# Optimization experiments

Measured on AMD Instinct MI355X. Metric: run time of the kernel, lower is better.

The kernel has to match this reference:

```python
import jax, jax.numpy as jnp
import numpy as np

EPS = 1e-08
MARGIN = 0.5
B, D = 512, 768
N_CLASSES = 7


def setup_inputs() -> dict:
    key = jax.random.key(0)
    k1, k2 = jax.random.split(key)
    embeddings = jax.random.normal(k1, (B, D), dtype=jnp.float32)
    labels = jax.random.randint(k2, (B,), 0, N_CLASSES, dtype=jnp.int64)
    return {"embeddings": embeddings, "labels": labels}


def _cosine_distance_matrix(x):
    # 1 - x_i . x_j / (max(||x_i||, eps) * max(||x_j||, eps))  (torch cosine_similarity semantics)
    norms = jnp.maximum(jnp.linalg.norm(x, axis=-1, keepdims=True), EPS)
    xn = x / norms
    return 1.0 - xn @ xn.T  # (B, B)


def _triplet_mask(labels):
    n = labels.shape[0]
    ne = ~jnp.eye(n, dtype=bool)  # indices not equal
    distinct = ne[:, :, None] & ne[:, None, :] & ne[None, :, :]  # i!=j, i!=k, j!=k
    lbl_eq = labels[None, :] == labels[:, None]  # (B, B)
    valid = lbl_eq[:, :, None] & ~lbl_eq[:, None, :]  # label[i]==label[j], label[i]!=label[k]
    return distinct & valid


def reference(embeddings, labels):
    dist = _cosine_distance_matrix(embeddings)  # (B, B)
    # triplet_loss[i, j, k] = d(i, j) - d(i, k) + margin
    tl = dist[:, :, None] - dist[:, None, :] + MARGIN  # (B, B, B)
    mask = _triplet_mask(labels)
    tl = jax.nn.relu(tl * mask.astype(tl.dtype))
    num_pos = jnp.sum((tl > EPS).astype(jnp.float32))
    return jnp.sum(tl) / (num_pos + EPS)
```

## Files before the change

### kernel.cpp

```cpp
#include <hip/hip_runtime.h>

#define EPSF 1e-8f
#define MARGINF 0.5f
#define BN 512
#define DD 768
#define BT 64
#define SPLITK 8
#define KC (DD / SPLITK)
#define LPAD 104
#define NORMBLK 128

typedef __attribute__((ext_vector_type(8))) short bf16x8;
typedef __attribute__((ext_vector_type(4))) float f32x4;

__device__ __forceinline__ short f2bf(float f) {
    unsigned int u = __float_as_uint(f);
    return (short)((u + 0x7FFFu + ((u >> 16) & 1u)) >> 16);
}

__device__ __forceinline__ bf16x8 pack8(const float4& a, const float4& b) {
    bf16x8 r;
    r[0] = f2bf(a.x); r[1] = f2bf(a.y); r[2] = f2bf(a.z); r[3] = f2bf(a.w);
    r[4] = f2bf(b.x); r[5] = f2bf(b.y); r[6] = f2bf(b.z); r[7] = f2bf(b.w);
    return r;
}

__global__ __launch_bounds__(256) void prep_kernel(const float* __restrict__ x,
                                                   float* __restrict__ invn,
                                                   float* __restrict__ dotp) {
    int b = blockIdx.x;
    int t = threadIdx.x;
    int wv = t >> 6, lane = t & 63;

    if (b >= BN) {
        int row = (b - BN) * 4 + wv;
        float s = 0.f;
#pragma unroll
        for (int c = 0; c < 3; ++c) {
            float4 v = *(const float4*)&x[row * DD + (lane + c * 64) * 4];
            s += v.x * v.x + v.y * v.y + v.z * v.z + v.w * v.w;
        }
        for (int off = 32; off; off >>= 1) s += __shfl_down(s, off, 64);
        if (lane == 0) invn[row] = 1.0f / fmaxf(sqrtf(s), EPSF);
        return;
    }

    __shared__ __align__(16) short As[BT][LPAD];
    __shared__ __align__(16) short Bs[BT][LPAD];
    int bz = b >> 6, bi = (b >> 3) & 7, bj = b & 7;
    int i0 = bi * BT, j0 = bj * BT, kbase = bz * KC;

    {
        int row = t >> 2, fq = t & 3;
        const float* ap = &x[(i0 + row) * DD + kbase + fq * 8];
        const float* bp = &x[(j0 + row) * DD + kbase + fq * 8];
#pragma unroll
        for (int cc = 0; cc < 3; ++cc) {
            float4 a0 = *(const float4*)(ap + cc * 32);
            float4 a1 = *(const float4*)(ap + cc * 32 + 4);
            float4 b0 = *(const float4*)(bp + cc * 32);
            float4 b1 = *(const float4*)(bp + cc * 32 + 4);
            *(bf16x8*)&As[row][fq * 8 + cc * 32] = pack8(a0, a1);
            *(bf16x8*)&Bs[row][fq * 8 + cc * 32] = pack8(b0, b1);
        }
    }
    __syncthreads();

    int r16 = lane & 15;
    int kb8 = (lane >> 4) * 8;

    f32x4 accf[4];
#pragma unroll
    for (int c = 0; c < 4; ++c) accf[c] = (f32x4){0.f, 0.f, 0.f, 0.f};

#pragma unroll
    for (int s = 0; s < 3; ++s) {
        bf16x8 af = *(const bf16x8*)&As[wv * 16 + r16][kb8 + s * 32];
#pragma unroll
        for (int c = 0; c < 4; ++c) {
            bf16x8 bf_ = *(const bf16x8*)&Bs[c * 16 + r16][kb8 + s * 32];
            accf[c] = __builtin_amdgcn_mfma_f32_16x16x32_bf16(af, bf_, accf[c], 0, 0, 0);
        }
    }

    float* o = dotp + (size_t)bz * BN * BN;
    int crow = i0 + wv * 16 + (lane >> 4) * 4;
#pragma unroll
    for (int c = 0; c < 4; ++c) {
        int ccol = j0 + c * 16 + r16;
#pragma unroll
        for (int r = 0; r < 4; ++r)
            o[(crow + r) * BN + ccol] = accf[c][r];
    }
}

__global__ __launch_bounds__(256) void triplet_kernel(const float* __restrict__ dotp,
                                                      const float* __restrict__ invn,
                                                      const int* __restrict__ labels,
                                                      float* __restrict__ psum,
                                                      unsigned int* __restrict__ pcnt) {
    int i = blockIdx.x;
    int t = threadIdx.x;
    int w = t >> 6, lane = t & 63;
    __shared__ float drow[BN];
    __shared__ int lab[BN];
    __shared__ __align__(16) float dpos[528];
    __shared__ int wcnt[8];
    __shared__ int woff[9];
    __shared__ float redf[4];
    __shared__ unsigned int redc[4];

    lab[t] = labels[t];
    lab[t + 256] = labels[t + 256];
    float inv_i = invn[i];
#pragma unroll
    for (int e0 = 0; e0 < BN; e0 += 256) {
        int e = e0 + t;
        float s = 0.f;
#pragma unroll
        for (int z = 0; z < SPLITK; ++z) s += dotp[(size_t)z * BN * BN + i * BN + e];
        drow[e] = 1.0f - s * inv_i * invn[e];
    }
    __syncthreads();

    int li = lab[i];
    bool p0 = (lab[t] == li) && (t != i);
    bool p1 = (lab[t + 256] == li) && ((t + 256) != i);
    unsigned long long m0 = __ballot(p0);
    unsigned long long m1 = __ballot(p1);
    if (lane == 0) { wcnt[w] = __popcll(m0); wcnt[4 + w] = __popcll(m1); }
    __syncthreads();
    if (t == 0) {
        int s = 0;
#pragma unroll
        for (int q = 0; q < 8; ++q) { woff[q] = s; s += wcnt[q]; }
        woff[8] = s;
    }
    __syncthreads();
    unsigned long long lmask = (1ull << lane) - 1ull;
    if (p0) dpos[woff[w] + __popcll(m0 & lmask)] = drow[t] + MARGINF;
    if (p1) dpos[woff[4 + w] + __popcll(m1 & lmask)] = drow[t + 256] + MARGINF;
    int npos = woff[8];
    int npad = (npos + 15) & ~15;
    if (t < npad - npos) dpos[npos + t] = -1e30f;
    __syncthreads();

    float dk0 = (lab[t] != li) ? drow[t] : 1e30f;
    float dk1 = (lab[t + 256] != li) ? drow[t + 256] : 1e30f;
    float sum = 0.f;
    unsigned int cnt = 0;
    for (int n = 0; n < npad; n += 16) {
        float4 q[4];
#pragma unroll
        for (int v = 0; v < 4; ++v) q[v] = *(const float4*)&dpos[n + v * 4];
#pragma unroll
        for (int v = 0; v < 4; ++v) {
            float bv[4] = {q[v].x, q[v].y, q[v].z, q[v].w};
#pragma unroll
            for (int u = 0; u < 4; ++u) {
                float v0 = bv[u] - dk0;
                float v1 = bv[u] - dk1;
                sum += fmaxf(v0, 0.f);
                if (v0 > EPSF) cnt++;
                sum += fmaxf(v1, 0.f);
                if (v1 > EPSF) cnt++;
            }
        }
    }
    for (int off = 32; off; off >>= 1) {
        sum += __shfl_down(sum, off, 64);
        cnt += __shfl_down(cnt, off, 64);
    }
    if (lane == 0) { redf[w] = sum; redc[w] = cnt; }
    __syncthreads();
    if (t == 0) {
        psum[i] = redf[0] + redf[1] + redf[2] + redf[3];
        pcnt[i] = redc[0] + redc[1] + redc[2] + redc[3];
    }
}

__global__ __launch_bounds__(256) void reduce_kernel(const float* __restrict__ psum,
                                                     const unsigned int* __restrict__ pcnt,
                                                     float* __restrict__ out) {
    int t = threadIdx.x;
    double s = (double)psum[t] + (double)psum[t + 256];
    double c = (double)pcnt[t] + (double)pcnt[t + 256];
    for (int off = 32; off; off >>= 1) {
        s += __shfl_down(s, off, 64);
        c += __shfl_down(c, off, 64);
    }
    __shared__ double sred[4], cred[4];
    if ((t & 63) == 0) { sred[t >> 6] = s; cred[t >> 6] = c; }
    __syncthreads();
    if (t == 0) {
        double stot = sred[0] + sred[1] + sred[2] + sred[3];
        double ctot = cred[0] + cred[1] + cred[2] + cred[3];
        out[0] = (float)(stot / (ctot + 1e-8));
    }
}

extern "C" void kernel_launch(void* const* d_in, const int* in_sizes, int n_in,
                              void* d_out, int out_size, void* d_ws, size_t ws_size,
                              hipStream_t stream) {
    const float* x = (const float*)d_in[0];
    const int* labels = (const int*)d_in[1];
    float* out = (float*)d_out;

    char* ws = (char*)d_ws;
    float* invn = (float*)(ws + 256);
    float* psum = (float*)(ws + 4096);
    unsigned int* pcnt = (unsigned int*)(ws + 8192);
    float* dotp = (float*)(ws + 16384);

    prep_kernel<<<BN + NORMBLK, 256, 0, stream>>>(x, invn, dotp);
    triplet_kernel<<<BN, 256, 0, stream>>>(dotp, invn, labels, psum, pcnt);
    reduce_kernel<<<1, 256, 0, stream>>>(psum, pcnt, out);
}
```

Before: 19.42 us.

## Replace split-K Gram partials with full-K 64x64 tiles in 1024-thread blocks

The Gram matrix kernel no longer splits K across 8 slices written to separate partial buffers. Each of 64 blocks of 1024 threads now loops over the full K dimension in 128-wide chunks and writes one final dot product per element. The triplet kernel then reads a single row instead of summing 8 partials, which cuts global write and read traffic by about 8x. The cost is far less GEMM parallelism (64 blocks instead of 512) and a serial K loop with two barriers per chunk and no prefetch overlap.

```diff
diff --git a/kernel.cpp b/kernel.cpp
--- a/kernel.cpp
+++ b/kernel.cpp
@@ -5,10 +5,11 @@
 #define BN 512
 #define DD 768
 #define BT 64
-#define SPLITK 8
-#define KC (DD / SPLITK)
-#define LPAD 104
-#define NORMBLK 128
+#define GBLK 64
+#define NBLK 32
+#define CHK 128
+#define NCHK 6
+#define LP 136
 
 typedef __attribute__((ext_vector_type(8))) short bf16x8;
 typedef __attribute__((ext_vector_type(4))) float f32x4;
@@ -25,15 +26,15 @@
     return r;
 }
 
-__global__ __launch_bounds__(256) void prep_kernel(const float* __restrict__ x,
-                                                   float* __restrict__ invn,
-                                                   float* __restrict__ dotp) {
+__global__ __launch_bounds__(1024) void prep_kernel(const float* __restrict__ x,
+                                                    float* __restrict__ invn,
+                                                    float* __restrict__ dist) {
     int b = blockIdx.x;
     int t = threadIdx.x;
     int wv = t >> 6, lane = t & 63;
 
-    if (b >= BN) {
-        int row = (b - BN) * 4 + wv;
+    if (b >= GBLK) {
+        int row = (b - GBLK) * 16 + wv;
         float s = 0.f;
 #pragma unroll
         for (int c = 0; c < 3; ++c) {
@@ -45,56 +46,45 @@
         return;
     }
 
-    __shared__ __align__(16) short As[BT][LPAD];
-    __shared__ __align__(16) short Bs[BT][LPAD];
-    int bz = b >> 6, bi = (b >> 3) & 7, bj = b & 7;
-    int i0 = bi * BT, j0 = bj * BT, kbase = bz * KC;
-
-    {
-        int row = t >> 2, fq = t & 3;
-        const float* ap = &x[(i0 + row) * DD + kbase + fq * 8];
-        const float* bp = &x[(j0 + row) * DD + kbase + fq * 8];
-#pragma unroll
-        for (int cc = 0; cc < 3; ++cc) {
-            float4 a0 = *(const float4*)(ap + cc * 32);
-            float4 a1 = *(const float4*)(ap + cc * 32 + 4);
-            float4 b0 = *(const float4*)(bp + cc * 32);
-            float4 b1 = *(const float4*)(bp + cc * 32 + 4);
-            *(bf16x8*)&As[row][fq * 8 + cc * 32] = pack8(a0, a1);
-            *(bf16x8*)&Bs[row][fq * 8 + cc * 32] = pack8(b0, b1);
+    __shared__ __align__(16) short As[BT][LP];
+    __shared__ __align__(16) short Bs[BT][LP];
+    int bi = b >> 3, bj = b & 7;
+    int i0 = bi * BT, j0 = bj * BT;
+
+    int wr = wv >> 2, wc = wv & 3;
+    int r16 = lane & 15, kb8 = (lane >> 4) * 8;
+    int srow = t >> 4, sf = (t & 15) * 8;
+
+    const float* arow = &x[(i0 + srow) * DD + sf];
+    const float* brow = &x[(j0 + srow) * DD + sf];
+
+    f32x4 acc = (f32x4){0.f, 0.f, 0.f, 0.f};
+    for (int c = 0; c < NCHK; ++c) {
+        int kb = c * CHK;
+        float4 a0 = *(const float4*)(arow + kb);
+        float4 a1 = *(const float4*)(arow + kb + 4);
+        float4 b0 = *(const float4*)(brow + kb);
+        float4 b1 = *(const float4*)(brow + kb + 4);
+        __syncthreads();
+        *(bf16x8*)&As[srow][sf] = pack8(a0, a1);
+        *(bf16x8*)&Bs[srow][sf] = pack8(b0, b1);
+        __syncthreads();
+#pragma unroll
+        for (int s = 0; s < 4; ++s) {
+            bf16x8 af = *(const bf16x8*)&As[wr * 16 + r16][kb8 + s * 32];
+            bf16x8 bf_ = *(const bf16x8*)&Bs[wc * 16 + r16][kb8 + s * 32];
+            acc = __builtin_amdgcn_mfma_f32_16x16x32_bf16(af, bf_, acc, 0, 0, 0);
         }
     }
-    __syncthreads();
-
-    int r16 = lane & 15;
-    int kb8 = (lane >> 4) * 8;
-
-    f32x4 accf[4];
-#pragma unroll
-    for (int c = 0; c < 4; ++c) accf[c] = (f32x4){0.f, 0.f, 0.f, 0.f};
-
-#pragma unroll
-    for (int s = 0; s < 3; ++s) {
-        bf16x8 af = *(const bf16x8*)&As[wv * 16 + r16][kb8 + s * 32];
-#pragma unroll
-        for (int c = 0; c < 4; ++c) {
-            bf16x8 bf_ = *(const bf16x8*)&Bs[c * 16 + r16][kb8 + s * 32];
-            accf[c] = __builtin_amdgcn_mfma_f32_16x16x32_bf16(af, bf_, accf[c], 0, 0, 0);
-        }
-    }
-
-    float* o = dotp + (size_t)bz * BN * BN;
-    int crow = i0 + wv * 16 + (lane >> 4) * 4;
-#pragma unroll
-    for (int c = 0; c < 4; ++c) {
-        int ccol = j0 + c * 16 + r16;
-#pragma unroll
-        for (int r = 0; r < 4; ++r)
-            o[(crow + r) * BN + ccol] = accf[c][r];
-    }
-}
-
-__global__ __launch_bounds__(256) void triplet_kernel(const float* __restrict__ dotp,
+
+    int crow = i0 + wr * 16 + (lane >> 4) * 4;
+    int ccol = j0 + wc * 16 + r16;
+#pragma unroll
+    for (int r = 0; r < 4; ++r)
+        dist[(crow + r) * BN + ccol] = acc[r];
+}
+
+__global__ __launch_bounds__(256) void triplet_kernel(const float* __restrict__ dist,
                                                       const float* __restrict__ invn,
                                                       const int* __restrict__ labels,
                                                       float* __restrict__ psum,
@@ -113,13 +103,11 @@
     lab[t] = labels[t];
     lab[t + 256] = labels[t + 256];
     float inv_i = invn[i];
-#pragma unroll
-    for (int e0 = 0; e0 < BN; e0 += 256) {
-        int e = e0 + t;
-        float s = 0.f;
-#pragma unroll
-        for (int z = 0; z < SPLITK; ++z) s += dotp[(size_t)z * BN * BN + i * BN + e];
-        drow[e] = 1.0f - s * inv_i * invn[e];
+    {
+        float2 iv = *(const float2*)&invn[2 * t];
+        float2 p = *(const float2*)&dist[i * BN + 2 * t];
+        drow[2 * t]     = 1.0f - p.x * inv_i * iv.x;
+        drow[2 * t + 1] = 1.0f - p.y * inv_i * iv.y;
     }
     __syncthreads();
 
@@ -210,9 +198,9 @@
     float* invn = (float*)(ws + 256);
     float* psum = (float*)(ws + 4096);
     unsigned int* pcnt = (unsigned int*)(ws + 8192);
-    float* dotp = (float*)(ws + 16384);
-
-    prep_kernel<<<BN + NORMBLK, 256, 0, stream>>>(x, invn, dotp);
-    triplet_kernel<<<BN, 256, 0, stream>>>(dotp, invn, labels, psum, pcnt);
+    float* dist = (float*)(ws + 16384);
+
+    prep_kernel<<<GBLK + NBLK, 1024, 0, stream>>>(x, invn, dist);
+    triplet_kernel<<<BN, 256, 0, stream>>>(dist, invn, labels, psum, pcnt);
     reduce_kernel<<<1, 256, 0, stream>>>(psum, pcnt, out);
 }
```

Measured after the change: 19.66 us. Within noise of the previous version (+1.2%).
